# Kernel tuning notes

Measured on AMD Instinct MI355X. Metric: run time of the kernel, lower is better.

The kernel has to match this reference:

```python
import jax, jax.numpy as jnp
import numpy as np

BN_EPS = 1e-5


def setup_inputs() -> dict:
    key = jax.random.key(0)
    ks = jax.random.split(key, 8)
    B, S, D = 2048, 64, 128      # batch, seq_len, d_in
    H, DK = 8, 16                # n_head, d_k; H*DK == 128
    F = H * DK
    std = np.sqrt(2.0 / DK).astype(np.float32)
    return {
        "v": jax.random.normal(ks[0], (B, S, D), jnp.float32),
        "Wq": jax.random.normal(ks[1], (F, D), jnp.float32) * std,
        "bq": jnp.zeros((F,), jnp.float32),
        "bn_gamma": jnp.ones((F,), jnp.float32),
        "bn_beta": jnp.zeros((F,), jnp.float32),
        "W2": jax.random.normal(ks[2], (F, F), jnp.float32) * (1.0 / np.sqrt(F)),
        "b2": jnp.zeros((F,), jnp.float32),
        "Wk": jax.random.normal(ks[3], (F, D), jnp.float32) * std,
        "bk": jnp.zeros((F,), jnp.float32),
    }


def reference(v, Wq, bq, bn_gamma, bn_beta, W2, b2, Wk, bk):
    # v: [B, S, D]
    B, S, D = v.shape
    F = Wq.shape[0]
    H = 8
    DK = F // H
    temperature = jnp.asarray(np.sqrt(DK), v.dtype)

    # q path: linear -> mean over seq -> BatchNorm1d (batch stats) -> linear
    q = jnp.einsum("bsd,fd->bsf", v, Wq) + bq          # [B, S, F]
    q = q.mean(axis=1)                                  # [B, F]
    mu = q.mean(axis=0)
    var = q.var(axis=0)                                 # biased, as BN uses
    q = (q - mu) * jax.lax.rsqrt(var + BN_EPS) * bn_gamma + bn_beta
    q = jnp.einsum("bf,gf->bg", q, W2) + b2             # [B, F]
    q = q.reshape(B, H, DK).transpose(1, 0, 2)          # [H, B, DK]

    # k path
    k = (jnp.einsum("bsd,fd->bsf", v, Wk) + bk).reshape(B, S, H, DK)
    k = k.transpose(2, 0, 1, 3)                         # [H, B, S, DK]

    # single query per (head, batch): scores over seq
    attn = jnp.einsum("hbd,hbsd->hbs", q, k) / temperature
    attn = jax.nn.softmax(attn, axis=-1)                # [H, B, S]
    # dropout is identity in eval mode

    # weighted sum over seq of the ORIGINAL v (torch repeats v per head;
    # broadcasting avoids materializing the repeat)
    out = jnp.einsum("hbs,bsd->hbd", attn, v)           # [H, B, D]
    return out, attn
```

## Files before the change

### kernel.cpp

```cpp
#include <hip/hip_runtime.h>

#define B_ 2048
#define S_ 64
#define D_ 128
#define F_ 128
#define H_ 8

__global__ __launch_bounds__(256) void k_q1(const float* __restrict__ v,
                                            const float* __restrict__ Wq,
                                            const float* __restrict__ bq,
                                            float* __restrict__ q1,
                                            float* __restrict__ gsum) {
  const int b = blockIdx.x;
  const int t = threadIdx.x;
  if (b == 0) gsum[t] = 0.f;

  __shared__ float red[8 * 128];
  __shared__ __align__(16) float vbarL[128];

  const int c4 = t & 31;
  const int r0 = t >> 5;
  const float4* v4 = (const float4*)(v + (size_t)b * (S_ * D_));
  float4 acc = {0.f, 0.f, 0.f, 0.f};
  #pragma unroll
  for (int i = 0; i < 8; ++i) {
    float4 x = v4[(r0 * 8 + i) * 32 + c4];
    acc.x += x.x; acc.y += x.y; acc.z += x.z; acc.w += x.w;
  }
  red[r0 * 128 + c4 * 4 + 0] = acc.x;
  red[r0 * 128 + c4 * 4 + 1] = acc.y;
  red[r0 * 128 + c4 * 4 + 2] = acc.z;
  red[r0 * 128 + c4 * 4 + 3] = acc.w;
  __syncthreads();
  if (t < 128) {
    float s = 0.f;
    #pragma unroll
    for (int r = 0; r < 8; ++r) s += red[r * 128 + t];
    vbarL[t] = s * (1.0f / 64.0f);
  }
  __syncthreads();

  const float4* Wq4 = (const float4*)Wq;
  const float4* vb4 = (const float4*)vbarL;
  const int d4 = t & 31;
  const int fg = t >> 5;
  #pragma unroll
  for (int fi = 0; fi < 16; ++fi) {
    int f = fi * 8 + fg;
    float4 w = Wq4[f * 32 + d4];
    float4 vv = vb4[d4];
    float p = w.x * vv.x + w.y * vv.y + w.z * vv.z + w.w * vv.w;
    #pragma unroll
    for (int off = 16; off; off >>= 1) p += __shfl_down(p, off, 32);
    if (d4 == 0) q1[b * F_ + f] = p + bq[f];
  }
}

__global__ __launch_bounds__(256) void k_stats2(const float* __restrict__ q1,
                                                const float* __restrict__ W2,
                                                float* __restrict__ gsum,
                                                float* __restrict__ gsq,
                                                float* __restrict__ W2t) {
  const int blk = blockIdx.x;
  const int t = threadIdx.x;
  const int f4 = t & 31, rg = t >> 5;
  const int r0 = blk * 32;
  const float4* q14 = (const float4*)q1;
  float4 s = {0.f, 0.f, 0.f, 0.f};
  float4 q = {0.f, 0.f, 0.f, 0.f};
  #pragma unroll
  for (int k = 0; k < 4; ++k) {
    float4 x = q14[(size_t)(r0 + rg + 8 * k) * 32 + f4];
    s.x += x.x; s.y += x.y; s.z += x.z; s.w += x.w;
    q.x += x.x * x.x; q.y += x.y * x.y; q.z += x.z * x.z; q.w += x.w * x.w;
  }
  __shared__ float rs[8][128], rq[8][128];
  rs[rg][f4 * 4 + 0] = s.x; rs[rg][f4 * 4 + 1] = s.y;
  rs[rg][f4 * 4 + 2] = s.z; rs[rg][f4 * 4 + 3] = s.w;
  rq[rg][f4 * 4 + 0] = q.x; rq[rg][f4 * 4 + 1] = q.y;
  rq[rg][f4 * 4 + 2] = q.z; rq[rg][f4 * 4 + 3] = q.w;
  __syncthreads();
  if (t < 128) {
    float ss = 0.f, qq = 0.f;
    #pragma unroll
    for (int r = 0; r < 8; ++r) { ss += rs[r][t]; qq += rq[r][t]; }
    atomicAdd(&gsum[t], ss);
    atomicAdd(&gsq[t], qq);
  }
  {
    int g = blk * 2 + (t >> 7);
    int f = t & 127;
    W2t[f * 128 + g] = W2[g * 128 + f];
  }
}

__global__ __launch_bounds__(256) void k_q2qw(const float* __restrict__ q1,
                                              const float* __restrict__ gsum,
                                              const float* __restrict__ gsq,
                                              const float* __restrict__ gamma,
                                              const float* __restrict__ beta,
                                              const float* __restrict__ W2t,
                                              const float* __restrict__ b2,
                                              const float* __restrict__ Wk,
                                              const float* __restrict__ bk,
                                              float* __restrict__ qW,
                                              float* __restrict__ qb) {
  const int b0 = blockIdx.x * 8;
  const int t = threadIdx.x;
  __shared__ float scaleL[128], shiftL[128];
  __shared__ __align__(16) float qnL[8 * 128];
  __shared__ __align__(16) float q2L[8 * 128];

  if (t < 128) {
    float mu = gsum[t] * (1.0f / (float)B_);
    float var = gsq[t] * (1.0f / (float)B_) - mu * mu;
    float rsg = rsqrtf(var + 1e-5f) * gamma[t];
    scaleL[t] = rsg;
    shiftL[t] = beta[t] - mu * rsg;
  }
  __syncthreads();
  {
    int row = t >> 5, f4 = t & 31;
    float4 x = ((const float4*)q1)[(size_t)(b0 + row) * 32 + f4];
    x.x = x.x * scaleL[f4 * 4 + 0] + shiftL[f4 * 4 + 0];
    x.y = x.y * scaleL[f4 * 4 + 1] + shiftL[f4 * 4 + 1];
    x.z = x.z * scaleL[f4 * 4 + 2] + shiftL[f4 * 4 + 2];
    x.w = x.w * scaleL[f4 * 4 + 3] + shiftL[f4 * 4 + 3];
    ((float4*)qnL)[row * 32 + f4] = x;
  }
  __syncthreads();

  {
    const int r = t >> 5, g4 = t & 31;
    const float4* W2t4 = (const float4*)W2t;
    float4 acc = ((const float4*)b2)[g4];
    #pragma unroll 8
    for (int f = 0; f < 128; ++f) {
      float4 w = W2t4[f * 32 + g4];
      float qv = qnL[r * 128 + f];
      acc.x += qv * w.x; acc.y += qv * w.y; acc.z += qv * w.z; acc.w += qv * w.w;
    }
    ((float4*)q2L)[r * 32 + g4] = acc;
  }
  __syncthreads();

  const float4* Wk4 = (const float4*)Wk;
  #pragma unroll
  for (int i = 0; i < 8; ++i) {
    int o4 = i * 256 + t;
    int bi = o4 >> 8, h = (o4 >> 5) & 7, d4 = o4 & 31;
    float4 acc = {0.f, 0.f, 0.f, 0.f};
    const float* q2row = &q2L[bi * 128 + h * 16];
    #pragma unroll
    for (int dk = 0; dk < 16; ++dk) {
      float qv = q2row[dk];
      float4 w = Wk4[(h * 16 + dk) * 32 + d4];
      acc.x += qv * w.x; acc.y += qv * w.y; acc.z += qv * w.z; acc.w += qv * w.w;
    }
    ((float4*)qW)[(size_t)(b0 + bi) * 256 + h * 32 + d4] = acc;
  }
  if (t < 64) {
    int bi = t >> 3, h = t & 7;
    float acc = 0.f;
    #pragma unroll
    for (int dk = 0; dk < 16; ++dk)
      acc += q2L[bi * 128 + h * 16 + dk] * bk[h * 16 + dk];
    qb[(b0 + bi) * 8 + h] = acc;
  }
}

__global__ __launch_bounds__(256) void k_attn(const float* __restrict__ v,
                                              const float* __restrict__ qW,
                                              const float* __restrict__ qb,
                                              float* __restrict__ outp) {
  const int b = blockIdx.x;
  const int t = threadIdx.x;
  __shared__ __align__(16) float vL[64 * 128];
  __shared__ __align__(16) float qWL[8 * 128];
  __shared__ float attnL[8 * 64];
  __shared__ float qbL[8];

  float4* vL4 = (float4*)vL;
  const float4* vg4 = (const float4*)(v + (size_t)b * (S_ * D_));
  #pragma unroll
  for (int i = 0; i < 8; ++i) {
    int idx = i * 256 + t;
    int s = idx >> 5, c4 = idx & 31;
    vL4[s * 32 + (c4 ^ (s & 31))] = vg4[idx];
  }
  {
    const float4* qWg4 = (const float4*)(qW + (size_t)b * (H_ * D_));
    ((float4*)qWL)[t] = qWg4[t];
  }
  if (t < 8) qbL[t] = qb[b * 8 + t];
  __syncthreads();

  const int s = t & 63;
  const int hq = t >> 6;
  const int h0 = hq * 2, h1 = hq * 2 + 1;
  const float4* qWL4 = (const float4*)qWL;
  float a0 = 0.f, a1 = 0.f;
  #pragma unroll
  for (int d4 = 0; d4 < 32; ++d4) {
    float4 vv = vL4[s * 32 + (d4 ^ (s & 31))];
    float4 w0 = qWL4[h0 * 32 + d4];
    float4 w1 = qWL4[h1 * 32 + d4];
    a0 += vv.x * w0.x + vv.y * w0.y + vv.z * w0.z + vv.w * w0.w;
    a1 += vv.x * w1.x + vv.y * w1.y + vv.z * w1.z + vv.w * w1.w;
  }
  float l0 = (a0 + qbL[h0]) * 0.25f;
  float l1 = (a1 + qbL[h1]) * 0.25f;

  float m0 = l0, m1 = l1;
  #pragma unroll
  for (int off = 32; off; off >>= 1) {
    m0 = fmaxf(m0, __shfl_xor(m0, off, 64));
    m1 = fmaxf(m1, __shfl_xor(m1, off, 64));
  }
  float e0 = __expf(l0 - m0), e1 = __expf(l1 - m1);
  float s0 = e0, s1 = e1;
  #pragma unroll
  for (int off = 32; off; off >>= 1) {
    s0 += __shfl_xor(s0, off, 64);
    s1 += __shfl_xor(s1, off, 64);
  }
  float at0 = e0 / s0, at1 = e1 / s1;
  attnL[h0 * 64 + s] = at0;
  attnL[h1 * 64 + s] = at1;
  float* attn_out = outp + (size_t)H_ * B_ * D_;
  attn_out[(size_t)h0 * (B_ * S_) + b * S_ + s] = at0;
  attn_out[(size_t)h1 * (B_ * S_) + b * S_ + s] = at1;
  __syncthreads();

  const int d4o = t & 31;
  const int h = t >> 5;
  float4 acc = {0.f, 0.f, 0.f, 0.f};
  #pragma unroll
  for (int si = 0; si < 64; ++si) {
    float a = attnL[h * 64 + si];
    float4 vv = vL4[si * 32 + (d4o ^ (si & 31))];
    acc.x += a * vv.x; acc.y += a * vv.y; acc.z += a * vv.z; acc.w += a * vv.w;
  }
  ((float4*)outp)[(size_t)h * (B_ * 32) + b * 32 + d4o] = acc;
}

extern "C" void kernel_launch(void* const* d_in, const int* in_sizes, int n_in,
                              void* d_out, int out_size, void* d_ws, size_t ws_size,
                              hipStream_t stream) {
  const float* v     = (const float*)d_in[0];
  const float* Wq    = (const float*)d_in[1];
  const float* bq    = (const float*)d_in[2];
  const float* gamma = (const float*)d_in[3];
  const float* beta  = (const float*)d_in[4];
  const float* W2    = (const float*)d_in[5];
  const float* b2    = (const float*)d_in[6];
  const float* Wk    = (const float*)d_in[7];
  const float* bk    = (const float*)d_in[8];

  float* ws = (float*)d_ws;
  float* q1v  = ws;
  float* gsum = q1v + (size_t)B_ * F_;
  float* gsq  = gsum + 128;
  float* W2t  = gsq + 128;
  float* qWv  = W2t + 128 * 128;
  float* qbv  = qWv + (size_t)B_ * H_ * D_;
  float* outp = (float*)d_out;

  hipLaunchKernelGGL(k_q1,     dim3(B_),  dim3(256), 0, stream, v, Wq, bq, q1v, gsum);
  hipLaunchKernelGGL(k_stats2, dim3(64),  dim3(256), 0, stream, q1v, W2, gsum, gsq, W2t);
  hipLaunchKernelGGL(k_q2qw,   dim3(256), dim3(256), 0, stream, q1v, gsum, gsq,
                     gamma, beta, W2t, b2, Wk, bk, qWv, qbv);
  hipLaunchKernelGGL(k_attn,   dim3(B_),  dim3(256), 0, stream, v, qWv, qbv, outp);
}
```

Measured before the change: 71.38 us.

## Process one batch row per block in q2/qW kernel with split-K reduction

The q2qw kernel now launches one block per batch row instead of one block per eight rows, giving 2048 blocks rather than 256. The W2 matvec is split across eight thread groups along the input dimension, and the partial sums are combined in shared memory. This is meant to fill more of the GPU's compute units and shorten each block's serial loop. In exchange, each block reloads W2t and Wk (more L2 traffic per output row) and pays an extra reduction step and barrier.

```diff
diff --git a/kernel.cpp b/kernel.cpp
--- a/kernel.cpp
+++ b/kernel.cpp
@@ -105,67 +105,64 @@
                                               const float* __restrict__ bk,
                                               float* __restrict__ qW,
                                               float* __restrict__ qb) {
-  const int b0 = blockIdx.x * 8;
-  const int t = threadIdx.x;
-  __shared__ float scaleL[128], shiftL[128];
-  __shared__ __align__(16) float qnL[8 * 128];
-  __shared__ __align__(16) float q2L[8 * 128];
+  const int b = blockIdx.x;
+  const int t = threadIdx.x;
+  __shared__ __align__(16) float qnL[128];
+  __shared__ __align__(16) float4 part4[256];
+  __shared__ __align__(16) float q2L[128];
 
   if (t < 128) {
     float mu = gsum[t] * (1.0f / (float)B_);
     float var = gsq[t] * (1.0f / (float)B_) - mu * mu;
     float rsg = rsqrtf(var + 1e-5f) * gamma[t];
-    scaleL[t] = rsg;
-    shiftL[t] = beta[t] - mu * rsg;
-  }
-  __syncthreads();
-  {
-    int row = t >> 5, f4 = t & 31;
-    float4 x = ((const float4*)q1)[(size_t)(b0 + row) * 32 + f4];
-    x.x = x.x * scaleL[f4 * 4 + 0] + shiftL[f4 * 4 + 0];
-    x.y = x.y * scaleL[f4 * 4 + 1] + shiftL[f4 * 4 + 1];
-    x.z = x.z * scaleL[f4 * 4 + 2] + shiftL[f4 * 4 + 2];
-    x.w = x.w * scaleL[f4 * 4 + 3] + shiftL[f4 * 4 + 3];
-    ((float4*)qnL)[row * 32 + f4] = x;
-  }
-  __syncthreads();
-
-  {
-    const int r = t >> 5, g4 = t & 31;
+    qnL[t] = q1[(size_t)b * F_ + t] * rsg + (beta[t] - mu * rsg);
+  }
+  __syncthreads();
+
+  {
+    const int fq = t >> 5, g4 = t & 31;
     const float4* W2t4 = (const float4*)W2t;
-    float4 acc = ((const float4*)b2)[g4];
-    #pragma unroll 8
-    for (int f = 0; f < 128; ++f) {
+    float4 p = {0.f, 0.f, 0.f, 0.f};
+    #pragma unroll
+    for (int k = 0; k < 16; ++k) {
+      int f = fq * 16 + k;
+      float qv = qnL[f];
       float4 w = W2t4[f * 32 + g4];
-      float qv = qnL[r * 128 + f];
-      acc.x += qv * w.x; acc.y += qv * w.y; acc.z += qv * w.z; acc.w += qv * w.w;
+      p.x += qv * w.x; p.y += qv * w.y; p.z += qv * w.z; p.w += qv * w.w;
     }
-    ((float4*)q2L)[r * 32 + g4] = acc;
-  }
-  __syncthreads();
-
-  const float4* Wk4 = (const float4*)Wk;
-  #pragma unroll
-  for (int i = 0; i < 8; ++i) {
-    int o4 = i * 256 + t;
-    int bi = o4 >> 8, h = (o4 >> 5) & 7, d4 = o4 & 31;
+    part4[fq * 32 + g4] = p;
+  }
+  __syncthreads();
+  if (t < 32) {
+    float4 acc = ((const float4*)b2)[t];
+    #pragma unroll
+    for (int r = 0; r < 8; ++r) {
+      float4 p = part4[r * 32 + t];
+      acc.x += p.x; acc.y += p.y; acc.z += p.z; acc.w += p.w;
+    }
+    ((float4*)q2L)[t] = acc;
+  }
+  __syncthreads();
+
+  {
+    const int h = t >> 5, d4 = t & 31;
+    const float4* Wk4 = (const float4*)Wk;
+    const float* q2row = &q2L[h * 16];
     float4 acc = {0.f, 0.f, 0.f, 0.f};
-    const float* q2row = &q2L[bi * 128 + h * 16];
     #pragma unroll
     for (int dk = 0; dk < 16; ++dk) {
       float qv = q2row[dk];
       float4 w = Wk4[(h * 16 + dk) * 32 + d4];
       acc.x += qv * w.x; acc.y += qv * w.y; acc.z += qv * w.z; acc.w += qv * w.w;
     }
-    ((float4*)qW)[(size_t)(b0 + bi) * 256 + h * 32 + d4] = acc;
-  }
-  if (t < 64) {
-    int bi = t >> 3, h = t & 7;
+    ((float4*)qW)[(size_t)b * 256 + h * 32 + d4] = acc;
+  }
+  if (t < 8) {
     float acc = 0.f;
     #pragma unroll
     for (int dk = 0; dk < 16; ++dk)
-      acc += q2L[bi * 128 + h * 16 + dk] * bk[h * 16 + dk];
-    qb[(b0 + bi) * 8 + h] = acc;
+      acc += q2L[t * 16 + dk] * bk[t * 16 + dk];
+    qb[b * 8 + t] = acc;
   }
 }
 
@@ -268,7 +265,7 @@
 
   hipLaunchKernelGGL(k_q1,     dim3(B_),  dim3(256), 0, stream, v, Wq, bq, q1v, gsum);
   hipLaunchKernelGGL(k_stats2, dim3(64),  dim3(256), 0, stream, q1v, W2, gsum, gsq, W2t);
-  hipLaunchKernelGGL(k_q2qw,   dim3(256), dim3(256), 0, stream, q1v, gsum, gsq,
+  hipLaunchKernelGGL(k_q2qw,   dim3(B_),  dim3(256), 0, stream, q1v, gsum, gsq,
                      gamma, beta, W2t, b2, Wk, bk, qWv, qbv);
   hipLaunchKernelGGL(k_attn,   dim3(B_),  dim3(256), 0, stream, v, qWv, qbv, outp);
 }
```

After: 62.15 us. 1.15x faster.
